# Kernel tuning notes

Hardware: AMD Instinct MI355X
Metric: run time of the kernel (lower is better)

The kernel has to match this reference:

```python
import jax, jax.numpy as jnp
import numpy as np

RES = (256, 256)
FLOW_TEMP_REG = 1e-3
LOSS_SCALING = True
EPS = 1e-9


def get_interpolation(events, flow, tref, res):
    # events: [B,N,4] (ts,y,x,p); flow: [B,N,2] per-event (flow_y, flow_x)
    warped = events[:, :, 1:3] + (tref - events[:, :, 0:1]) * flow  # [B,N,2] (y,x)
    top_y = jnp.floor(warped[:, :, 0:1])
    bot_y = top_y + 1.0
    left_x = jnp.floor(warped[:, :, 1:2])
    right_x = left_x + 1.0
    # four bilinear corners stacked along the event dim -> [B,4N,2]
    idx = jnp.concatenate([
        jnp.concatenate([top_y, left_x], axis=2),
        jnp.concatenate([top_y, right_x], axis=2),
        jnp.concatenate([bot_y, left_x], axis=2),
        jnp.concatenate([bot_y, right_x], axis=2)], axis=1)
    w = jnp.maximum(0.0, 1.0 - jnp.abs(jnp.tile(warped, (1, 4, 1)) - idx))  # [B,4N,2]
    mask = ((idx[:, :, 0:1] >= 0) & (idx[:, :, 0:1] < res[0]) &
            (idx[:, :, 1:2] >= 0) & (idx[:, :, 1:2] < res[1])).astype(w.dtype)
    idx = idx * mask  # out-of-bounds -> pixel 0 with zero weight
    w = w * mask
    flat_idx = (idx[:, :, 0] * res[1] + idx[:, :, 1]).astype(jnp.int32)  # [B,4N]
    weights = w[:, :, 0] * w[:, :, 1]  # bilinear weight, [B,4N]
    return flat_idx, weights


def interpolate(flat_idx, w, npix):
    # per-batch scatter-add of weights into a flat pixel grid -> [B, H*W]
    return jax.vmap(lambda i, v: jax.ops.segment_sum(v, i, num_segments=npix))(flat_idx, w)


def scale_loss(iwe_pos, iwe_neg, iwe_pos_ts, iwe_neg_ts):
    loss = jnp.sum(iwe_pos_ts ** 2, axis=1) + jnp.sum(iwe_neg_ts ** 2, axis=1)  # [B]
    if LOSS_SCALING:
        nonzero_px = jnp.sum(((iwe_pos + iwe_neg) != 0).astype(loss.dtype), axis=1)
        loss = loss / (nonzero_px + EPS)
    return jnp.sum(loss)


def forward(event_list, flow, pol_mask, vector_list, max_ts):
    res = RES
    npix = res[0] * res[1]
    mt = jnp.asarray(max_ts, jnp.float32)
    pm = jnp.tile(pol_mask, (1, 4, 1))                    # [B,4N,2]
    ts4 = jnp.tile(event_list[:, :, 0], (1, 4))           # [B,4N]
    loss = jnp.float32(0.0)
    # forward warp (tref=max_ts, weight ts) and backward warp (tref=0, weight max_ts-ts)
    for tref, ts_w in ((mt, ts4), (jnp.float32(0.0), mt - ts4)):
        idx, w = get_interpolation(event_list, flow, tref, res)
        wp = w * pm[:, :, 0]
        wn = w * pm[:, :, 1]
        iwe_pos = interpolate(idx, wp, npix)
        iwe_neg = interpolate(idx, wn, npix)
        iwe_pos_ts = interpolate(idx, wp * ts_w, npix) / (iwe_pos + EPS) / mt
        iwe_neg_ts = interpolate(idx, wn * ts_w, npix) / (iwe_neg + EPS) / mt
        loss = loss + scale_loss(iwe_pos, iwe_neg, iwe_pos_ts, iwe_neg_ts)
    # single flow scale in _flow_list -> divide by 1
    loss = loss / 1.0
    # Charbonnier temporal smoothness on flow vectors [B,P,8]
    dt = vector_list[:, :-1, :] - vector_list[:, 1:, :]
    dt = jnp.sqrt(dt ** 2 + EPS).reshape(vector_list.shape[0], -1)
    loss = loss + FLOW_TEMP_REG * jnp.sum(jnp.mean(dt, axis=1))
    return loss


def setup_inputs() -> dict:
    B, N, P = 8, 262144, 4
    H, W = RES
    key = jax.random.key(0)
    ks = jax.random.split(key, 6)
    ts = jax.random.uniform(ks[0], (B, N, 1), dtype=jnp.float32) * P
    y = jax.random.uniform(ks[1], (B, N, 1), dtype=jnp.float32) * (H - 1)
    x = jax.random.uniform(ks[2], (B, N, 1), dtype=jnp.float32) * (W - 1)
    p = jax.random.bernoulli(ks[3], 0.5, (B, N, 1)).astype(jnp.float32) * 2.0 - 1.0
    event_list = jnp.concatenate([ts, y, x, p], axis=2)
    pos = (p > 0).astype(jnp.float32)
    pol_mask = jnp.concatenate([pos, 1.0 - pos], axis=2)
    flow = jax.random.normal(ks[4], (B, N, 2), dtype=jnp.float32) * 2.0
    vector_list = jax.random.normal(ks[5], (B, P, 8), dtype=jnp.float32)
    return {"event_list": event_list, "flow": flow, "pol_mask": pol_mask,
            "vector_list": vector_list, "max_ts": P}


def reference(event_list, flow, pol_mask, vector_list, max_ts):
    return forward(event_list, flow, pol_mask, vector_list, max_ts)
```

## Files before the change

### kernel.cpp

```cpp
#include <hip/hip_runtime.h>
#include <math.h>

#define RES_H 256
#define RES_W 256
#define EPSF 1e-9f
#define FLOW_TEMP_REG 1e-3f

#define BAND_SHIFT 4
#define BAND_ROWS 16
#define N_BANDS 16
#define BAND_PX (BAND_ROWS * RES_W)
#define CAP 24576
#define QS 2048.0f
#define QINV (1.0f / 2048.0f)
#define EV_PER_BLOCK 2048
#define EV_PER_THREAD 8

#define PAD 32

typedef unsigned long long u64;
typedef unsigned int u32;

__device__ __forceinline__ float decode_mt(const int* p) {
    int raw = *p;
    if (raw >= 0 && raw < (1 << 23)) return (float)raw;
    union { int i; float f; } u; u.i = raw; return u.f;
}



__global__ void __launch_bounds__(256) ew_bin(
    const float4* __restrict__ ev, const float2* __restrict__ flow,
    const int* __restrict__ mt_ptr, u64* __restrict__ recs,
    u32* __restrict__ counts, int N)
{
    __shared__ u32 hist[32], basebuf[32], cursor[32];
    const int b = blockIdx.y;
    const int start = blockIdx.x * EV_PER_BLOCK;
    const int tid = threadIdx.x;
    if (tid < 32) { hist[tid] = 0u; cursor[tid] = 0u; }
    __syncthreads();

    const float mt = decode_mt(mt_ptr);
    const float inv_mt = 1.0f / mt;

    u64 rc[EV_PER_THREAD][2];
    u32 vm = 0u;
    #pragma unroll
    for (int j = 0; j < EV_PER_THREAD; ++j) {
        int i = start + tid + j * 256;
        float4 e; float2 f;
        if (i < N) { e = ev[b * N + i]; f = flow[b * N + i]; }
        else { e = make_float4(0.f, -100.f, -100.f, 1.f); f = make_float2(0.f, 0.f); }
        #pragma unroll
        for (int dir = 0; dir < 2; ++dir) {
            float dtt = (dir ? 0.0f : mt) - e.x;
            float tswn = (dir ? (mt - e.x) : e.x) * inv_mt;
            float wy = fminf(fmaxf(e.y + dtt * f.x, -8.0f), 264.0f);
            float wx = fminf(fmaxf(e.z + dtt * f.y, -8.0f), 264.0f);
            int wyf = __float2int_rn(wy * 4096.0f);
            int wxf = __float2int_rn(wx * 4096.0f);
            int iy = wyf >> 12, ix = wxf >> 12;
            if (iy < -1 || iy > 255 || ix < -1 || ix > 255) continue;
            u32 tq = __float2uint_rn(fminf(fmaxf(tswn, 0.0f), 1.0f) * 4096.0f);
            rc[j][dir] = (u64)((u32)wyf & 0x3FFFFFu)
                       | ((u64)((u32)wxf & 0x3FFFFFu) << 22)
                       | ((u64)tq << 44)
                       | ((u64)(e.w > 0.0f ? 0u : 1u) << 57);
            vm |= 1u << (j * 2 + dir);
            int t1 = iy >> BAND_SHIFT;
            int t2 = (iy + 1) >> BAND_SHIFT;
            if (t1 >= 0) atomicAdd(&hist[dir * 16 + t1], 1u);
            if (t2 <= 15 && t2 != t1) atomicAdd(&hist[dir * 16 + t2], 1u);
        }
    }
    __syncthreads();
    if (tid < 32) basebuf[tid] = atomicAdd(&counts[(b * 32 + tid) * PAD], hist[tid]);
    __syncthreads();

    #pragma unroll
    for (int j = 0; j < EV_PER_THREAD; ++j) {
        #pragma unroll
        for (int dir = 0; dir < 2; ++dir) {
            if (!(vm & (1u << (j * 2 + dir)))) continue;
            u64 rec = rc[j][dir];
            int iy = ((int)(((u32)rec & 0x3FFFFFu) << 10)) >> 22;
            int t1 = iy >> BAND_SHIFT;
            int t2 = (iy + 1) >> BAND_SHIFT;
            #pragma unroll
            for (int s = 0; s < 2; ++s) {
                int t = s ? t2 : t1;
                if (t < 0 || t > 15) continue;
                if (s && t2 == t1) continue;
                int k = dir * 16 + t;
                u32 off = atomicAdd(&cursor[k], 1u);
                u32 slot = basebuf[k] + off;
                if (slot >= CAP) slot = CAP - 1;
                recs[(size_t)(b * 32 + k) * CAP + slot] = rec;
            }
        }
    }
}

__global__ void __launch_bounds__(1024) ew_accum(
    const u64* __restrict__ recs, const u32* __restrict__ counts,
    float* __restrict__ partials, const float* __restrict__ vec,
    float* __restrict__ out, int B, int P)
{
    __shared__ u32 lds[2 * BAND_PX];
    __shared__ float wterm[16], wnz[16];
    __shared__ int is_last_s;
    const int band = blockIdx.x, bd = blockIdx.y;
    const int q = bd * 16 + band;
    const int row0 = band << BAND_SHIFT;
    const int tid = threadIdx.x;
    for (int i = tid; i < 2 * BAND_PX; i += 1024) lds[i] = 0u;
    __syncthreads();

    u32 cnt = counts[q * PAD]; if (cnt > CAP) cnt = CAP;
    const u64* bucket = recs + (size_t)q * CAP;

    for (u32 i = tid; i < cnt; i += 1024) {
        u64 rec = bucket[i];
        int wyf = ((int)(((u32)rec & 0x3FFFFFu) << 10)) >> 10;
        int wxf = ((int)(((u32)(rec >> 22) & 0x3FFFFFu) << 10)) >> 10;
        float tswn = (float)((u32)(rec >> 44) & 0x1FFFu) * (1.0f / 4096.0f);
        u32 pol = (u32)(rec >> 57) & 1u;
        int ry = (wyf >> 12) - row0;
        int ix = wxf >> 12;
        float fy = (float)(wyf & 0xFFF) * (1.0f / 4096.0f);
        float fx = (float)(wxf & 0xFFF) * (1.0f / 4096.0f);
        u32* pl = lds + pol * BAND_PX;
        #pragma unroll
        for (int cc = 0; cc < 4; ++cc) {
            int cy = ry + (cc >> 1), cx = ix + (cc & 1);
            if ((unsigned)cy >= BAND_ROWS || (unsigned)cx >= RES_W) continue;
            float wgt = ((cc >> 1) ? fy : 1.0f - fy) * ((cc & 1) ? fx : 1.0f - fx);
            u32 v = (__float2uint_rn(wgt * tswn * QS) << 16)
                  |  __float2uint_rn(wgt * QS);
            if (v) atomicAdd(&pl[(cy << 8) | cx], v);
        }
    }
    __syncthreads();

    const uint4 pp = ((const uint4*)lds)[tid];
    const uint4 nn = ((const uint4*)(lds + BAND_PX))[tid];
    const u32 pu[4] = {pp.x, pp.y, pp.z, pp.w};
    const u32 nu[4] = {nn.x, nn.y, nn.z, nn.w};
    float term = 0.0f, nz = 0.0f;
    #pragma unroll
    for (int j = 0; j < 4; ++j) {
        u32 wp_r = pu[j] & 0xFFFFu, tp_r = pu[j] >> 16;
        u32 wn_r = nu[j] & 0xFFFFu, tn_r = nu[j] >> 16;
        float wp = (float)wp_r * QINV, tp = (float)tp_r * QINV;
        float wn = (float)wn_r * QINV, tn = (float)tn_r * QINV;
        float pts = tp / (wp + EPSF);
        float nts = tn / (wn + EPSF);
        term += pts * pts + nts * nts;
        nz   += ((wp_r | wn_r) != 0u) ? 1.0f : 0.0f;
    }
    #pragma unroll
    for (int off = 32; off > 0; off >>= 1) {
        term += __shfl_down(term, off);
        nz   += __shfl_down(nz, off);
    }
    if ((tid & 63) == 0) { wterm[tid >> 6] = term; wnz[tid >> 6] = nz; }
    __syncthreads();

    u32* done  = (u32*)(partials + 512);
    u32* done2 = (u32*)(partials + 1024);
    if (tid == 0) {
        float t = 0.0f, z = 0.0f;
        #pragma unroll
        for (int wv = 0; wv < 16; ++wv) { t += wterm[wv]; z += wnz[wv]; }
        atomicAdd(&partials[bd * PAD + 0], t);
        atomicAdd(&partials[bd * PAD + 1], z);
        __threadfence();
        int last = 0;
        if (atomicAdd(&done[bd * PAD], 1u) == N_BANDS - 1u) {
            if (atomicAdd(done2, 1u) == 15u) last = 1;
        }
        is_last_s = last;
    }
    __syncthreads();
    if (!is_last_s) return;

    __threadfence();
    float v = 0.0f;
    if (tid < 16) {
        float s = __hip_atomic_load(&partials[tid * PAD + 0],
                                    __ATOMIC_RELAXED, __HIP_MEMORY_SCOPE_AGENT);
        float n = __hip_atomic_load(&partials[tid * PAD + 1],
                                    __ATOMIC_RELAXED, __HIP_MEMORY_SCOPE_AGENT);
        v = s / (n + EPSF);
    }
    const int per_b = (P - 1) * 8;
    const int tot = B * per_b;
    float sm = 0.0f;
    for (int i = tid; i < tot; i += 1024) {
        int bb = i / per_b;
        int r = i - bb * per_b;
        int pi = r >> 3, j = r & 7;
        float d = vec[(bb * P + pi) * 8 + j] - vec[(bb * P + pi + 1) * 8 + j];
        sm += sqrtf(d * d + EPSF);
    }
    float val = v + sm / (float)per_b * FLOW_TEMP_REG;
    #pragma unroll
    for (int off = 32; off > 0; off >>= 1) val += __shfl_down(val, off);
    if ((tid & 63) == 0) wterm[tid >> 6] = val;
    __syncthreads();
    if (tid == 0) {
        float t = 0.0f;
        #pragma unroll
        for (int wv = 0; wv < 16; ++wv) t += wterm[wv];
        out[0] = t;
    }
}

extern "C" void kernel_launch(void* const* d_in, const int* in_sizes, int n_in,
                              void* d_out, int out_size, void* d_ws, size_t ws_size,
                              hipStream_t stream) {
    const float4* ev   = (const float4*)d_in[0];
    const float2* flow = (const float2*)d_in[1];
    const float*  vec  = (const float*)d_in[3];
    const int*    mtp  = (const int*)d_in[4];

    const int B = 8;
    const int N = in_sizes[0] / (B * 4);
    const int P = in_sizes[3] / (B * 8);

    float* partials = (float*)((char*)d_ws + 32768);
    u32*   counts   = (u32*)d_ws;
    u64*   recs     = (u64*)((char*)d_ws + 65536);

    hipMemsetAsync(d_ws, 0, 65536, stream);

    dim3 bgrid((N + EV_PER_BLOCK - 1) / EV_PER_BLOCK, B);
    ew_bin<<<bgrid, 256, 0, stream>>>(ev, flow, mtp, recs, counts, N);

    dim3 agrid(N_BANDS, 16);
    ew_accum<<<agrid, 1024, 0, stream>>>(recs, counts, partials, vec,
                                         (float*)d_out, B, P);
}
```

Measured before the change: 132.6 us.

## Pack binned event records into 32 bits with coarser quantisation

Binned per-event records shrink from 64-bit to 32-bit words. They now hold a band-relative row, column, 6-bit sub-pixel fractions, a 5-bit time weight and polarity. The binning pass keeps the raw event and flow loads in registers and recomputes the warp in its second loop instead of storing packed records. This halves the scatter-write and gather-read traffic through global memory, at the cost of much coarser bilinear and time-weight quantisation, which may hurt accuracy.

```diff
diff --git a/kernel.cpp b/kernel.cpp
--- a/kernel.cpp
+++ b/kernel.cpp
@@ -31,7 +31,7 @@
 
 __global__ void __launch_bounds__(256) ew_bin(
     const float4* __restrict__ ev, const float2* __restrict__ flow,
-    const int* __restrict__ mt_ptr, u64* __restrict__ recs,
+    const int* __restrict__ mt_ptr, u32* __restrict__ recs,
     u32* __restrict__ counts, int N)
 {
     __shared__ u32 hist[32], basebuf[32], cursor[32];
@@ -44,30 +44,24 @@
     const float mt = decode_mt(mt_ptr);
     const float inv_mt = 1.0f / mt;
 
-    u64 rc[EV_PER_THREAD][2];
-    u32 vm = 0u;
+    float4 e[EV_PER_THREAD];
+    float2 f[EV_PER_THREAD];
     #pragma unroll
     for (int j = 0; j < EV_PER_THREAD; ++j) {
         int i = start + tid + j * 256;
-        float4 e; float2 f;
-        if (i < N) { e = ev[b * N + i]; f = flow[b * N + i]; }
-        else { e = make_float4(0.f, -100.f, -100.f, 1.f); f = make_float2(0.f, 0.f); }
+        if (i < N) { e[j] = ev[b * N + i]; f[j] = flow[b * N + i]; }
+        else { e[j] = make_float4(0.f, -100.f, -100.f, 1.f); f[j] = make_float2(0.f, 0.f); }
+    }
+
+    #pragma unroll
+    for (int j = 0; j < EV_PER_THREAD; ++j) {
         #pragma unroll
         for (int dir = 0; dir < 2; ++dir) {
-            float dtt = (dir ? 0.0f : mt) - e.x;
-            float tswn = (dir ? (mt - e.x) : e.x) * inv_mt;
-            float wy = fminf(fmaxf(e.y + dtt * f.x, -8.0f), 264.0f);
-            float wx = fminf(fmaxf(e.z + dtt * f.y, -8.0f), 264.0f);
-            int wyf = __float2int_rn(wy * 4096.0f);
-            int wxf = __float2int_rn(wx * 4096.0f);
-            int iy = wyf >> 12, ix = wxf >> 12;
+            float dtt = (dir ? 0.0f : mt) - e[j].x;
+            float wy = fminf(fmaxf(e[j].y + dtt * f[j].x, -8.0f), 264.0f);
+            float wx = fminf(fmaxf(e[j].z + dtt * f[j].y, -8.0f), 264.0f);
+            int iy = (int)floorf(wy), ix = (int)floorf(wx);
             if (iy < -1 || iy > 255 || ix < -1 || ix > 255) continue;
-            u32 tq = __float2uint_rn(fminf(fmaxf(tswn, 0.0f), 1.0f) * 4096.0f);
-            rc[j][dir] = (u64)((u32)wyf & 0x3FFFFFu)
-                       | ((u64)((u32)wxf & 0x3FFFFFu) << 22)
-                       | ((u64)tq << 44)
-                       | ((u64)(e.w > 0.0f ? 0u : 1u) << 57);
-            vm |= 1u << (j * 2 + dir);
             int t1 = iy >> BAND_SHIFT;
             int t2 = (iy + 1) >> BAND_SHIFT;
             if (t1 >= 0) atomicAdd(&hist[dir * 16 + t1], 1u);
@@ -82,9 +76,18 @@
     for (int j = 0; j < EV_PER_THREAD; ++j) {
         #pragma unroll
         for (int dir = 0; dir < 2; ++dir) {
-            if (!(vm & (1u << (j * 2 + dir)))) continue;
-            u64 rec = rc[j][dir];
-            int iy = ((int)(((u32)rec & 0x3FFFFFu) << 10)) >> 22;
+            float dtt = (dir ? 0.0f : mt) - e[j].x;
+            float tswn = (dir ? (mt - e[j].x) : e[j].x) * inv_mt;
+            float wy = fminf(fmaxf(e[j].y + dtt * f[j].x, -8.0f), 264.0f);
+            float wx = fminf(fmaxf(e[j].z + dtt * f[j].y, -8.0f), 264.0f);
+            float tyf = floorf(wy), txf = floorf(wx);
+            int iy = (int)tyf, ix = (int)txf;
+            if (iy < -1 || iy > 255 || ix < -1 || ix > 255) continue;
+            u32 fy6 = __float2uint_rn((wy - tyf) * 63.0f);
+            u32 fx6 = __float2uint_rn((wx - txf) * 63.0f);
+            u32 tq  = __float2uint_rn(fminf(fmaxf(tswn, 0.0f), 1.0f) * 31.0f);
+            u32 base = ((u32)(ix + 1) << 5) | (fy6 << 14) | (fx6 << 20)
+                     | (tq << 26) | ((e[j].w > 0.0f ? 0u : 1u) << 31);
             int t1 = iy >> BAND_SHIFT;
             int t2 = (iy + 1) >> BAND_SHIFT;
             #pragma unroll
@@ -96,14 +99,15 @@
                 u32 off = atomicAdd(&cursor[k], 1u);
                 u32 slot = basebuf[k] + off;
                 if (slot >= CAP) slot = CAP - 1;
-                recs[(size_t)(b * 32 + k) * CAP + slot] = rec;
+                recs[(size_t)(b * 32 + k) * CAP + slot] =
+                    base | (u32)(iy + 1 - (t << BAND_SHIFT));
             }
         }
     }
 }
 
 __global__ void __launch_bounds__(1024) ew_accum(
-    const u64* __restrict__ recs, const u32* __restrict__ counts,
+    const u32* __restrict__ recs, const u32* __restrict__ counts,
     float* __restrict__ partials, const float* __restrict__ vec,
     float* __restrict__ out, int B, int P)
 {
@@ -112,25 +116,21 @@
     __shared__ int is_last_s;
     const int band = blockIdx.x, bd = blockIdx.y;
     const int q = bd * 16 + band;
-    const int row0 = band << BAND_SHIFT;
     const int tid = threadIdx.x;
     for (int i = tid; i < 2 * BAND_PX; i += 1024) lds[i] = 0u;
     __syncthreads();
 
     u32 cnt = counts[q * PAD]; if (cnt > CAP) cnt = CAP;
-    const u64* bucket = recs + (size_t)q * CAP;
+    const u32* bucket = recs + (size_t)q * CAP;
 
     for (u32 i = tid; i < cnt; i += 1024) {
-        u64 rec = bucket[i];
-        int wyf = ((int)(((u32)rec & 0x3FFFFFu) << 10)) >> 10;
-        int wxf = ((int)(((u32)(rec >> 22) & 0x3FFFFFu) << 10)) >> 10;
-        float tswn = (float)((u32)(rec >> 44) & 0x1FFFu) * (1.0f / 4096.0f);
-        u32 pol = (u32)(rec >> 57) & 1u;
-        int ry = (wyf >> 12) - row0;
-        int ix = wxf >> 12;
-        float fy = (float)(wyf & 0xFFF) * (1.0f / 4096.0f);
-        float fx = (float)(wxf & 0xFFF) * (1.0f / 4096.0f);
-        u32* pl = lds + pol * BAND_PX;
+        u32 rec = bucket[i];
+        int ry = (int)(rec & 31u) - 1;
+        int ix = (int)((rec >> 5) & 511u) - 1;
+        float fy = (float)((rec >> 14) & 63u) * (1.0f / 63.0f);
+        float fx = (float)((rec >> 20) & 63u) * (1.0f / 63.0f);
+        float tswn = (float)((rec >> 26) & 31u) * (1.0f / 31.0f);
+        u32* pl = lds + (rec >> 31) * BAND_PX;
         #pragma unroll
         for (int cc = 0; cc < 4; ++cc) {
             int cy = ry + (cc >> 1), cx = ix + (cc & 1);
@@ -229,9 +229,9 @@
     const int N = in_sizes[0] / (B * 4);
     const int P = in_sizes[3] / (B * 8);
 
+    u32*   counts   = (u32*)d_ws;
     float* partials = (float*)((char*)d_ws + 32768);
-    u32*   counts   = (u32*)d_ws;
-    u64*   recs     = (u64*)((char*)d_ws + 65536);
+    u32*   recs     = (u32*)((char*)d_ws + 65536);
 
     hipMemsetAsync(d_ws, 0, 65536, stream);
 
```

Result: slower. 136.8 us (+3.1%).
